# Optimization experiments

Hardware: AMD Instinct MI355X
Metric: run time of the kernel (lower is better)

## Reference

```python
import jax, jax.numpy as jnp
import numpy as np
import math

N_HEADS = 8
EMBED = 128
HEAD_DEPTH = EMBED // N_HEADS
CLIP = 10.0
NEG_INF = 1.0e10
SCALE = math.sqrt(HEAD_DEPTH)


def setup_inputs() -> dict:
    key = jax.random.key(0)
    ks = jax.random.split(key, 8)
    B, C, N = 32, 2, 512
    Q = jax.random.normal(ks[0], (B, C, N, EMBED), dtype=jnp.float32)
    K = jax.random.normal(ks[1], (B, C, N, EMBED), dtype=jnp.float32)
    V = jax.random.normal(ks[2], (B, C, N, EMBED), dtype=jnp.float32)
    mask = jax.random.bernoulli(ks[3], 0.15, (B, C, N, 1))  # True = masked out
    stdv_qkv = 1.0 / math.sqrt(HEAD_DEPTH)
    stdv_out = 1.0 / math.sqrt(EMBED)
    # torch nn.Linear weights: (out_features, in_features)
    Wq = jax.random.uniform(ks[4], (EMBED, EMBED), jnp.float32, -stdv_qkv, stdv_qkv)
    Wk = jax.random.uniform(ks[5], (EMBED, EMBED), jnp.float32, -stdv_qkv, stdv_qkv)
    Wv = jax.random.uniform(ks[6], (EMBED, EMBED), jnp.float32, -stdv_qkv, stdv_qkv)
    Wout = jax.random.uniform(ks[7], (EMBED, EMBED), jnp.float32, -stdv_out, stdv_out)
    return {"Q": Q, "K": K, "V": V, "mask": mask,
            "Wq": Wq, "Wk": Wk, "Wv": Wv, "Wout": Wout}


def _split_heads(T):
    # (b, c, n, E) -> (b, H, c, n, d)
    b, c, n, _ = T.shape
    return T.reshape(b, c, n, N_HEADS, HEAD_DEPTH).transpose(0, 3, 1, 2, 4)


def reference(Q, K, V, mask, Wq, Wk, Wv, Wout):
    # Linear projections (torch Linear: y = x @ W.T)
    q = _split_heads(jnp.einsum('bcne,fe->bcnf', Q, Wq))
    k = _split_heads(jnp.einsum('bcne,fe->bcnf', K, Wk))
    v = _split_heads(jnp.einsum('bcne,fe->bcnf', V, Wv))
    # logits: (b, H, c, q, k)
    logits = jnp.einsum('bhcqd,bhckd->bhcqk', q, k) / SCALE
    logits = CLIP * jnp.tanh(logits)
    # mask (b, c, n, 1) -> (b, 1, c, 1, n); True -> -1e10
    m = mask[:, None, :, :, :].swapaxes(-1, -2)
    logits = jnp.where(m, -NEG_INF, logits)
    probs = jax.nn.softmax(logits, axis=-1)
    out = jnp.einsum('bhcqk,bhckd->bhcqd', probs, v)
    # combine heads: (b, H, c, n, d) -> (b, c, n, E)
    b, h, c, n, d = out.shape
    out = out.transpose(0, 2, 3, 1, 4).reshape(b, c, n, EMBED)
    return jnp.einsum('bcne,fe->bcnf', out, Wout)
```

## Files before the change

kernel.cpp:

```cpp
#include <hip/hip_runtime.h>

typedef _Float16 half_t;
typedef _Float16 half8 __attribute__((ext_vector_type(8)));
typedef _Float16 half4 __attribute__((ext_vector_type(4)));
typedef float floatx4 __attribute__((ext_vector_type(4)));
typedef float floatx16 __attribute__((ext_vector_type(16)));

#define C1 0.72134752044448170368f
#define C2 14.4269504088896340736f
#define C3 28.8539008177792681472f

__device__ __forceinline__ floatx4 zero4() {
    floatx4 z; z[0] = z[1] = z[2] = z[3] = 0.f; return z;
}
__device__ __forceinline__ floatx16 zero16() {
    floatx16 z;
#pragma unroll
    for (int i = 0; i < 16; ++i) z[i] = 0.f;
    return z;
}

__device__ __forceinline__ float pfun(float sp, float b) {
    float u = __builtin_amdgcn_exp2f(sp);
    float r = __builtin_amdgcn_rcpf(u + 1.0f);
    return __builtin_amdgcn_exp2f(b - C3 * r);
}

__global__ void k_convw(const float* __restrict__ Wq, const float* __restrict__ Wk,
                        const float* __restrict__ Wv, const float* __restrict__ Wo,
                        half_t* __restrict__ Wh) {
    int idx = blockIdx.x * 256 + threadIdx.x;
    int which = idx >> 14;
    int off = idx & 16383;
    const float* src = (which == 0) ? Wq : (which == 1) ? Wk : (which == 2) ? Wv : Wo;
    float scale = (which == 0) ? C1 : 1.0f;
    Wh[idx] = (half_t)(src[off] * scale);
}

__global__ __launch_bounds__(256) void k_proj(
        const float* __restrict__ Q, const float* __restrict__ K,
        const float* __restrict__ V, const half_t* __restrict__ WhBase,
        half_t* __restrict__ qw, half_t* __restrict__ kw, half_t* __restrict__ vw) {
    int which = blockIdx.y;
    const float* X = (which == 0) ? Q : (which == 1) ? K : V;
    const half_t* W = WhBase + which * 16384;

    int tid = threadIdx.x;
    int w = tid >> 6, lane = tid & 63;
    int l15 = lane & 15, quad = lane >> 4;
    int tokbase = blockIdx.x * 64 + w * 16;

    floatx4 acc[8];
#pragma unroll
    for (int nt = 0; nt < 8; ++nt) acc[nt] = zero4();

#pragma unroll
    for (int ks = 0; ks < 4; ++ks) {
        const float* ap = X + (tokbase + l15) * 128 + ks * 32 + quad * 8;
        float4 a0 = *(const float4*)ap;
        float4 a1 = *(const float4*)(ap + 4);
        half8 xf;
        xf[0] = (half_t)a0.x; xf[1] = (half_t)a0.y; xf[2] = (half_t)a0.z; xf[3] = (half_t)a0.w;
        xf[4] = (half_t)a1.x; xf[5] = (half_t)a1.y; xf[6] = (half_t)a1.z; xf[7] = (half_t)a1.w;
        if (which == 2) {
#pragma unroll
            for (int nt = 0; nt < 8; ++nt) {
                half8 wf = *(const half8*)(W + (nt * 16 + l15) * 128 + ks * 32 + quad * 8);
                acc[nt] = __builtin_amdgcn_mfma_f32_16x16x32_f16(xf, wf, acc[nt], 0, 0, 0);
            }
        } else {
#pragma unroll
            for (int nt = 0; nt < 8; ++nt) {
                half8 wf = *(const half8*)(W + (nt * 16 + l15) * 128 + ks * 32 + quad * 8);
                acc[nt] = __builtin_amdgcn_mfma_f32_16x16x32_f16(wf, xf, acc[nt], 0, 0, 0);
            }
        }
    }

    if (which == 2) {
        int R0 = tokbase + quad * 4;
        int bc = R0 >> 9, n0 = R0 & 511;
#pragma unroll
        for (int nt = 0; nt < 8; ++nt) {
            half4 hv;
            hv[0] = (half_t)acc[nt][0]; hv[1] = (half_t)acc[nt][1];
            hv[2] = (half_t)acc[nt][2]; hv[3] = (half_t)acc[nt][3];
            *(half4*)(vw + ((bc * 8 + nt) * 16 + l15) * 512 + n0) = hv;
        }
    } else {
        int R = tokbase + l15;
        int bc = R >> 9, n = R & 511;
        half_t* Y = (which == 0) ? qw : kw;
#pragma unroll
        for (int nt = 0; nt < 8; ++nt) {
            half4 hv;
            hv[0] = (half_t)acc[nt][0]; hv[1] = (half_t)acc[nt][1];
            hv[2] = (half_t)acc[nt][2]; hv[3] = (half_t)acc[nt][3];
            *(half4*)(Y + ((bc * 8 + nt) * 512 + n) * 16 + quad * 4) = hv;
        }
    }
}

__global__ __launch_bounds__(64, 4) void k_attn(
        const half_t* __restrict__ qg, const half_t* __restrict__ kg,
        const half_t* __restrict__ vTg, const int* __restrict__ mask,
        half_t* __restrict__ attn) {
    __shared__ float bias[512];
    __shared__ half_t Pb[32 * 36];

    int bx = blockIdx.x;
    int bch = bx >> 4, qt = bx & 15;
    int bc = bch >> 3, h = bch & 7;
    int lane = threadIdx.x;
    int l31 = lane & 31, hf = lane >> 5;
    int l15 = lane & 15, quad = lane >> 4;

    const half_t* qh = qg + bch * 8192;
    const half_t* kh = kg + bch * 8192;
    const half_t* vh = vTg + bch * 8192;

#pragma unroll
    for (int i = 0; i < 8; ++i)
        bias[i * 64 + lane] = mask[bc * 512 + i * 64 + lane] ? -1.0e30f : C2;
    __syncthreads();

    int qbase = qt * 32;
    half8 qf = *(const half8*)(qh + (qbase + l31) * 16 + hf * 8);

    half8 ones;
#pragma unroll
    for (int j = 0; j < 8; ++j) ones[j] = (half_t)1.0f;

    floatx4 O[2], Os[2];
    O[0] = zero4(); O[1] = zero4();
    Os[0] = zero4(); Os[1] = zero4();
    const float4* b4 = (const float4*)bias;

#pragma unroll 1
    for (int c = 0; c < 16; ++c) {
        half8 kf = *(const half8*)(kh + (c * 32 + l31) * 16 + hf * 8);
        half8 vf = *(const half8*)(vh + l15 * 512 + c * 32 + quad * 8);
        float4 bv[4];
#pragma unroll
        for (int g = 0; g < 4; ++g) bv[g] = b4[c * 8 + hf + 2 * g];

        floatx16 S = __builtin_amdgcn_mfma_f32_32x32x16_f16(kf, qf, zero16(), 0, 0, 0);
#pragma unroll
        for (int g = 0; g < 4; ++g) {
            float p0 = pfun(S[4 * g + 0], bv[g].x);
            float p1 = pfun(S[4 * g + 1], bv[g].y);
            float p2 = pfun(S[4 * g + 2], bv[g].z);
            float p3 = pfun(S[4 * g + 3], bv[g].w);
            auto t0 = __builtin_amdgcn_cvt_pkrtz(p0, p1);
            auto t1 = __builtin_amdgcn_cvt_pkrtz(p2, p3);
            half4 ph;
            ph[0] = (half_t)t0[0]; ph[1] = (half_t)t0[1];
            ph[2] = (half_t)t1[0]; ph[3] = (half_t)t1[1];
            *(half4*)(Pb + l31 * 36 + hf * 4 + g * 8) = ph;
        }
#pragma unroll
        for (int nt2 = 0; nt2 < 2; ++nt2) {
            half8 pb = *(const half8*)(Pb + (nt2 * 16 + l15) * 36 + quad * 8);
            O[nt2]  = __builtin_amdgcn_mfma_f32_16x16x32_f16(vf,   pb, O[nt2],  0, 0, 0);
            Os[nt2] = __builtin_amdgcn_mfma_f32_16x16x32_f16(ones, pb, Os[nt2], 0, 0, 0);
        }
    }

#pragma unroll
    for (int nt = 0; nt < 2; ++nt) {
        float iv = __builtin_amdgcn_rcpf(Os[nt][0]);
        int qrow = qbase + nt * 16 + l15;
        half4 ov;
        ov[0] = (half_t)(O[nt][0] * iv);
        ov[1] = (half_t)(O[nt][1] * iv);
        ov[2] = (half_t)(O[nt][2] * iv);
        ov[3] = (half_t)(O[nt][3] * iv);
        *(half4*)(attn + (bc * 512 + qrow) * 128 + h * 16 + quad * 4) = ov;
    }
}

__global__ __launch_bounds__(256) void k_out(
        const half_t* __restrict__ A, const half_t* __restrict__ Wh,
        float* __restrict__ out) {
    int tid = threadIdx.x;
    int w = tid >> 6, lane = tid & 63;
    int l15 = lane & 15, quad = lane >> 4;
    int tokbase = blockIdx.x * 64 + w * 16;

    floatx4 acc[8];
#pragma unroll
    for (int nt = 0; nt < 8; ++nt) acc[nt] = zero4();
#pragma unroll
    for (int ks = 0; ks < 4; ++ks) {
        half8 xf = *(const half8*)(A + (tokbase + l15) * 128 + ks * 32 + quad * 8);
#pragma unroll
        for (int nt = 0; nt < 8; ++nt) {
            half8 wf = *(const half8*)(Wh + (nt * 16 + l15) * 128 + ks * 32 + quad * 8);
            acc[nt] = __builtin_amdgcn_mfma_f32_16x16x32_f16(wf, xf, acc[nt], 0, 0, 0);
        }
    }
#pragma unroll
    for (int nt = 0; nt < 8; ++nt) {
        float4 o;
        o.x = acc[nt][0]; o.y = acc[nt][1]; o.z = acc[nt][2]; o.w = acc[nt][3];
        *(float4*)(out + (tokbase + l15) * 128 + nt * 16 + quad * 4) = o;
    }
}

extern "C" void kernel_launch(void* const* d_in, const int* in_sizes, int n_in,
                              void* d_out, int out_size, void* d_ws, size_t ws_size,
                              hipStream_t stream) {
    const float* Q    = (const float*)d_in[0];
    const float* K    = (const float*)d_in[1];
    const float* V    = (const float*)d_in[2];
    const int*   mask = (const int*)d_in[3];
    const float* Wq   = (const float*)d_in[4];
    const float* Wk   = (const float*)d_in[5];
    const float* Wv   = (const float*)d_in[6];
    const float* Wo   = (const float*)d_in[7];
    float* out = (float*)d_out;

    half_t* ws = (half_t*)d_ws;
    half_t* Wh = ws;
    half_t* qw = ws + 65536;
    half_t* kw = qw + 4194304;
    half_t* vw = kw + 4194304;
    half_t* aw = vw + 4194304;

    k_convw<<<256, 256, 0, stream>>>(Wq, Wk, Wv, Wo, Wh);
    k_proj<<<dim3(512, 3), 256, 0, stream>>>(Q, K, V, Wh, qw, kw, vw);
    k_attn<<<8192, 64, 0, stream>>>(qw, kw, vw, mask, aw);
    k_out<<<512, 256, 0, stream>>>(aw, Wh + 49152, out);
}
```

Baseline: 179.9 us.

## Software-pipeline attention loop with double-buffered P tiles in LDS

Restructures the key-chunk loop in k_attn into a two-stage software pipeline. The QK^T MFMA and exp/softmax work for chunk c+1 is interleaved with the PV MFMAs for chunk c, using two LDS P buffers in ping-pong. K and V fragments are prefetched one chunk ahead. The aim is to overlap transcendental ALU work with matrix ops and hide load latency, at the cost of more registers and LDS. Correctness relies on a single wave per block, since there are no barriers between LDS writes and reads.

```diff
diff --git a/kernel.cpp b/kernel.cpp
--- a/kernel.cpp
+++ b/kernel.cpp
@@ -101,12 +101,44 @@
     }
 }
 
+#define PSTORE_G(Sv, g, bvv, PW) do {                                      \
+    float p0 = pfun((Sv)[4*(g)+0], (bvv).x);                               \
+    float p1 = pfun((Sv)[4*(g)+1], (bvv).y);                               \
+    float p2 = pfun((Sv)[4*(g)+2], (bvv).z);                               \
+    float p3 = pfun((Sv)[4*(g)+3], (bvv).w);                               \
+    auto t0 = __builtin_amdgcn_cvt_pkrtz(p0, p1);                          \
+    auto t1 = __builtin_amdgcn_cvt_pkrtz(p2, p3);                          \
+    half4 ph;                                                              \
+    ph[0] = (half_t)t0[0]; ph[1] = (half_t)t0[1];                          \
+    ph[2] = (half_t)t1[0]; ph[3] = (half_t)t1[1];                          \
+    *(half4*)((PW) + (g) * 8) = ph;                                        \
+} while (0)
+
+#define PFUN_STORE(Sv, c, PW) do {                                         \
+    float4 bv0 = b4[(c) * 8 + hf + 0];                                     \
+    float4 bv1 = b4[(c) * 8 + hf + 2];                                     \
+    float4 bv2 = b4[(c) * 8 + hf + 4];                                     \
+    float4 bv3 = b4[(c) * 8 + hf + 6];                                     \
+    PSTORE_G(Sv, 0, bv0, PW);                                              \
+    PSTORE_G(Sv, 1, bv1, PW);                                              \
+    PSTORE_G(Sv, 2, bv2, PW);                                              \
+    PSTORE_G(Sv, 3, bv3, PW);                                              \
+} while (0)
+
+#define PV_STEP(p0v, p1v, vfv) do {                                        \
+    O[0]  = __builtin_amdgcn_mfma_f32_16x16x32_f16((vfv), (p0v), O[0], 0, 0, 0);  \
+    Os[0] = __builtin_amdgcn_mfma_f32_16x16x32_f16(ones,  (p0v), Os[0], 0, 0, 0); \
+    O[1]  = __builtin_amdgcn_mfma_f32_16x16x32_f16((vfv), (p1v), O[1], 0, 0, 0);  \
+    Os[1] = __builtin_amdgcn_mfma_f32_16x16x32_f16(ones,  (p1v), Os[1], 0, 0, 0); \
+} while (0)
+
 __global__ __launch_bounds__(64, 4) void k_attn(
         const half_t* __restrict__ qg, const half_t* __restrict__ kg,
         const half_t* __restrict__ vTg, const int* __restrict__ mask,
         half_t* __restrict__ attn) {
     __shared__ float bias[512];
-    __shared__ half_t Pb[32 * 36];
+    __shared__ half_t PbA[32 * 36];
+    __shared__ half_t PbB[32 * 36];
 
     int bx = blockIdx.x;
     int bch = bx >> 4, qt = bx & 15;
@@ -136,35 +168,47 @@
     Os[0] = zero4(); Os[1] = zero4();
     const float4* b4 = (const float4*)bias;
 
+    half_t* pwA = PbA + l31 * 36 + hf * 4;
+    half_t* pwB = PbB + l31 * 36 + hf * 4;
+    const half_t* prA0 = PbA + l15 * 36 + quad * 8;
+    const half_t* prA1 = prA0 + 16 * 36;
+    const half_t* prB0 = PbB + l15 * 36 + quad * 8;
+    const half_t* prB1 = prB0 + 16 * 36;
+
+    half8 kf = *(const half8*)(kh + l31 * 16 + hf * 8);
+    half8 vf = *(const half8*)(vh + l15 * 512 + quad * 8);
+    floatx16 S0 = __builtin_amdgcn_mfma_f32_32x32x16_f16(kf, qf, zero16(), 0, 0, 0);
+    kf = *(const half8*)(kh + (32 + l31) * 16 + hf * 8);
+    PFUN_STORE(S0, 0, pwA);
+
 #pragma unroll 1
-    for (int c = 0; c < 16; ++c) {
-        half8 kf = *(const half8*)(kh + (c * 32 + l31) * 16 + hf * 8);
-        half8 vf = *(const half8*)(vh + l15 * 512 + c * 32 + quad * 8);
-        float4 bv[4];
-#pragma unroll
-        for (int g = 0; g < 4; ++g) bv[g] = b4[c * 8 + hf + 2 * g];
-
-        floatx16 S = __builtin_amdgcn_mfma_f32_32x32x16_f16(kf, qf, zero16(), 0, 0, 0);
-#pragma unroll
-        for (int g = 0; g < 4; ++g) {
-            float p0 = pfun(S[4 * g + 0], bv[g].x);
-            float p1 = pfun(S[4 * g + 1], bv[g].y);
-            float p2 = pfun(S[4 * g + 2], bv[g].z);
-            float p3 = pfun(S[4 * g + 3], bv[g].w);
-            auto t0 = __builtin_amdgcn_cvt_pkrtz(p0, p1);
-            auto t1 = __builtin_amdgcn_cvt_pkrtz(p2, p3);
-            half4 ph;
-            ph[0] = (half_t)t0[0]; ph[1] = (half_t)t0[1];
-            ph[2] = (half_t)t1[0]; ph[3] = (half_t)t1[1];
-            *(half4*)(Pb + l31 * 36 + hf * 4 + g * 8) = ph;
-        }
-#pragma unroll
-        for (int nt2 = 0; nt2 < 2; ++nt2) {
-            half8 pb = *(const half8*)(Pb + (nt2 * 16 + l15) * 36 + quad * 8);
-            O[nt2]  = __builtin_amdgcn_mfma_f32_16x16x32_f16(vf,   pb, O[nt2],  0, 0, 0);
-            Os[nt2] = __builtin_amdgcn_mfma_f32_16x16x32_f16(ones, pb, Os[nt2], 0, 0, 0);
-        }
-    }
+    for (int t = 0; t < 7; ++t) {
+        int c1 = 2 * t + 1, c2 = 2 * t + 2;
+        floatx16 S1 = __builtin_amdgcn_mfma_f32_32x32x16_f16(kf, qf, zero16(), 0, 0, 0);
+        half8 kf2 = *(const half8*)(kh + (c2 * 32 + l31) * 16 + hf * 8);
+        half8 pa0 = *(const half8*)prA0;
+        half8 pa1 = *(const half8*)prA1;
+        half8 vfn = *(const half8*)(vh + l15 * 512 + c1 * 32 + quad * 8);
+        PFUN_STORE(S1, c1, pwB);
+        PV_STEP(pa0, pa1, vf);
+        floatx16 S2 = __builtin_amdgcn_mfma_f32_32x32x16_f16(kf2, qf, zero16(), 0, 0, 0);
+        kf = *(const half8*)(kh + ((c2 + 1) * 32 + l31) * 16 + hf * 8);
+        half8 pb0 = *(const half8*)prB0;
+        half8 pb1 = *(const half8*)prB1;
+        vf = *(const half8*)(vh + l15 * 512 + c2 * 32 + quad * 8);
+        PFUN_STORE(S2, c2, pwA);
+        PV_STEP(pb0, pb1, vfn);
+    }
+
+    floatx16 S15 = __builtin_amdgcn_mfma_f32_32x32x16_f16(kf, qf, zero16(), 0, 0, 0);
+    half8 pa0 = *(const half8*)prA0;
+    half8 pa1 = *(const half8*)prA1;
+    half8 vfn = *(const half8*)(vh + l15 * 512 + 15 * 32 + quad * 8);
+    PFUN_STORE(S15, 15, pwB);
+    PV_STEP(pa0, pa1, vf);
+    half8 pb0 = *(const half8*)prB0;
+    half8 pb1 = *(const half8*)prB1;
+    PV_STEP(pb0, pb1, vfn);
 
 #pragma unroll
     for (int nt = 0; nt < 2; ++nt) {
```

After: 182.5 us. Within noise of the previous version (+1.4%).
